# Performance work log

Hardware: AMD Instinct MI355X
Metric: run time of the kernel (lower is better)

Reference implementation:

```python
import jax, jax.numpy as jnp
import numpy as np

D_MODEL = 1024
EXPAND = 2
INNER = D_MODEL * EXPAND  # 2048
D_STATE = 64
K = 3
BSZ = 2
SEQ = 4096


def setup_inputs() -> dict:
    key = jax.random.key(0)
    ks = jax.random.split(key, 12)
    s = 0.02

    def w(k, shape):
        return jax.random.normal(k, shape, jnp.float32) * s

    return {
        "x": jax.random.normal(ks[0], (BSZ, SEQ, D_MODEL), jnp.float32),
        "W_in": w(ks[1], (D_MODEL, 2 * INNER)),
        "b_in": jnp.zeros((2 * INNER,), jnp.float32),
        "conv_w": w(ks[2], (INNER, K)),            # depthwise kernel per channel
        "conv_b": jnp.zeros((INNER,), jnp.float32),
        "W_dt": w(ks[3], (INNER, D_STATE)),
        "b_dt": jnp.zeros((D_STATE,), jnp.float32),
        "W_B": w(ks[4], (INNER, D_STATE)),
        "b_B": jnp.zeros((D_STATE,), jnp.float32),
        "W_C": w(ks[5], (INNER, D_STATE)),
        "b_C": jnp.zeros((D_STATE,), jnp.float32),
        "W_si": w(ks[6], (D_STATE, INNER)),
        "b_si": jnp.zeros((INNER,), jnp.float32),
        "D": jnp.ones((INNER,), jnp.float32),
        "W_out": w(ks[7], (INNER, D_MODEL)),
        "b_out": jnp.zeros((D_MODEL,), jnp.float32),
    }


def reference(x, W_in, b_in, conv_w, conv_b, W_dt, b_dt, W_B, b_B, W_C, b_C,
              W_si, b_si, D, W_out, b_out):
    bsz, seq_len, _ = x.shape
    inner = W_in.shape[1] // 2
    k = conv_w.shape[1]

    xz = x @ W_in + b_in                      # [B, L, 2*inner]
    x_main, gate = xz[..., :inner], xz[..., inner:]

    # Causal depthwise conv: torch pads k-1 both sides then slices [:L],
    # equivalent to left-pad (k-1), right-pad 0.
    lhs = jnp.transpose(x_main, (0, 2, 1))    # [B, C, L]
    rhs = conv_w[:, None, :]                  # [C, 1, K]
    conv = jax.lax.conv_general_dilated(
        lhs, rhs, window_strides=(1,), padding=[(k - 1, 0)],
        dimension_numbers=("NCH", "OIH", "NCH"), feature_group_count=inner)
    x_main = jnp.transpose(conv, (0, 2, 1)) + conv_b  # [B, L, inner]
    x_main = jax.nn.silu(x_main)

    dt = jax.nn.sigmoid(x_main @ W_dt + b_dt)  # [B, L, d_state]
    Bm = x_main @ W_B + b_B
    Cm = x_main @ W_C + b_C

    # Selective state recurrence: state_t = (1-dt_t)*state_{t-1} + dt_t*B_t
    def step(state, inp):
        dt_t, B_t, C_t = inp                  # each [B, d_state]
        state = (1.0 - dt_t) * state + dt_t * B_t
        return state, C_t * state

    xs = (jnp.moveaxis(dt, 1, 0), jnp.moveaxis(Bm, 1, 0), jnp.moveaxis(Cm, 1, 0))
    state0 = jnp.zeros((bsz, dt.shape[-1]), x.dtype)
    _, y = jax.lax.scan(step, state0, xs)     # [L, B, d_state]
    y = jnp.moveaxis(y, 0, 1)                 # [B, L, d_state]

    # LayerNorm over last dim, no affine, eps=1e-5 (torch F.layer_norm default)
    mu = jnp.mean(y, axis=-1, keepdims=True)
    var = jnp.var(y, axis=-1, keepdims=True)
    y = (y - mu) * jax.lax.rsqrt(var + 1e-5)

    y = y @ W_si + b_si                       # [B, L, inner]
    y = y + D * x_main
    y = y * jax.nn.sigmoid(gate)
    return y @ W_out + b_out                  # [B, L, d_model]
```

## Files before the change

### kernel.cpp

```cpp
#include <hip/hip_runtime.h>
#include <hip/hip_bf16.h>
#include <math.h>


namespace {

typedef __bf16 bf16x8 __attribute__((ext_vector_type(8)));
typedef float  f32x4  __attribute__((ext_vector_type(4)));
typedef unsigned short u16;

constexpr int kSeq = 4096;

__device__ __forceinline__ float sigmoid_f(float x) { return 1.0f / (1.0f + expf(-x)); }
__device__ __forceinline__ u16   f2bf(float f) { __bf16 h = (__bf16)f; return __builtin_bit_cast(u16, h); }
__device__ __forceinline__ float bf2f(u16 u)   { return (float)__builtin_bit_cast(__bf16, u); }

__device__ __forceinline__ void gll16(const u16* g, u16* l) {
    __builtin_amdgcn_global_load_lds(
        (const __attribute__((address_space(1))) unsigned int*)g,
        (__attribute__((address_space(3))) unsigned int*)l,
        16, 0, 0);
}

__device__ __forceinline__ int xcd_swizzle(int lin, int nwg) {
    const int q = nwg >> 3, r = nwg & 7;
    const int xcd = lin & 7, idx = lin >> 3;
    return (xcd < r ? xcd * (q + 1) : r * (q + 1) + (xcd - r) * q) + idx;
}

__global__ __launch_bounds__(256)
void convert_bf16(const float* __restrict__ in, u16* __restrict__ out, long n4)
{
    long i = (long)blockIdx.x * 256 + threadIdx.x;
    if (i >= n4) return;
    float4 v = reinterpret_cast<const float4*>(in)[i];
    ushort4 o = make_ushort4(f2bf(v.x), f2bf(v.y), f2bf(v.z), f2bf(v.w));
    reinterpret_cast<ushort4*>(out)[i] = o;
}

__device__ __forceinline__ void tr_body(float (*tile)[33],
                                        const float* __restrict__ in, u16* __restrict__ out,
                                        int R, int C, int r0, int c0, int t)
{
    const int lr = t >> 3, lc = (t & 7) * 4;
    float4 v = *reinterpret_cast<const float4*>(in + (size_t)(r0 + lr) * C + c0 + lc);
    tile[lr][lc + 0] = v.x; tile[lr][lc + 1] = v.y;
    tile[lr][lc + 2] = v.z; tile[lr][lc + 3] = v.w;
    __syncthreads();
    const int oc = t >> 3, orr = (t & 7) * 4;
    ushort4 o = make_ushort4(f2bf(tile[orr + 0][oc]), f2bf(tile[orr + 1][oc]),
                             f2bf(tile[orr + 2][oc]), f2bf(tile[orr + 3][oc]));
    *reinterpret_cast<ushort4*>(out + (size_t)(c0 + oc) * R + r0 + orr) = o;
}

__global__ __launch_bounds__(256)
void transpose_big(const float* __restrict__ Win, u16* __restrict__ WinT,
                   const float* __restrict__ Wout, u16* __restrict__ WoutT)
{
    __shared__ float tile[32][33];
    const int t = threadIdx.x;
    if (blockIdx.z == 0) {
        tr_body(tile, Win, WinT, 1024, 4096, blockIdx.y * 32, blockIdx.x * 32, t);
    } else {
        if (blockIdx.x >= 64) return;
        tr_body(tile, Wout, WoutT, 2048, 1024, blockIdx.x * 32, blockIdx.y * 32, t);
    }
}

__global__ __launch_bounds__(256)
void transpose_small(const float* __restrict__ Wdt, const float* __restrict__ WB,
                     const float* __restrict__ WC,  const float* __restrict__ Wsi,
                     u16* __restrict__ WdtbcT, u16* __restrict__ WsiT)
{
    __shared__ float tile[32][33];
    const int t = threadIdx.x;
    const int z = blockIdx.z;
    if (z < 3) {
        const float* in = (z == 0) ? Wdt : (z == 1) ? WB : WC;
        u16* out = WdtbcT + (size_t)z * 64 * 2048;
        tr_body(tile, in, out, 2048, 64, blockIdx.y * 32, blockIdx.x * 32, t);
    } else {
        tr_body(tile, Wsi, WsiT, 64, 2048, blockIdx.x * 32, blockIdx.y * 32, t);
    }
}

template <int BM, int BN, int EPI>
__global__ __launch_bounds__(256)
void gemm_mfma(const u16* __restrict__ A, const u16* __restrict__ Bt,
               const float* __restrict__ b0, const float* __restrict__ b1,
               const float* __restrict__ b2,
               const u16* __restrict__ aux0, const u16* __restrict__ aux1,
               void* __restrict__ o0, int N, int K, int nbx)
{
    constexpr int FM = BM / 32, FN = BN / 32;
    constexpr int CA = BM / 32, CB = BN / 32;
    __shared__ __align__(16) u16 As[BM][64];
    __shared__ __align__(16) u16 Bs[BN][64];

    const int tid  = threadIdx.x;
    const int lane = tid & 63;
    const int wid  = tid >> 6;
    const int wr   = (wid >> 1) * (BM / 2);
    const int wc   = (wid & 1)  * (BN / 2);
    const int swz  = xcd_swizzle(blockIdx.x, gridDim.x);
    const int row0 = (swz / nbx) * BM;
    const int col0 = (swz % nbx) * BN;

    const int srow = lane >> 3;
    const int scol = ((lane & 7) ^ srow) * 8;
    const int fr   = lane & 15;
    const int fq   = lane >> 4;

    f32x4 acc[FM][FN];
#pragma unroll
    for (int m = 0; m < FM; ++m)
#pragma unroll
        for (int n = 0; n < FN; ++n) acc[m][n] = (f32x4){0.f, 0.f, 0.f, 0.f};

    for (int k0 = 0; k0 < K; k0 += 64) {
#pragma unroll
        for (int i = 0; i < CA; ++i) {
            const int c = wid * CA + i;
            gll16(A + (size_t)(row0 + c * 8 + srow) * K + k0 + scol,
                  &As[0][0] + c * 512 + lane * 8);
        }
#pragma unroll
        for (int i = 0; i < CB; ++i) {
            const int c = wid * CB + i;
            gll16(Bt + (size_t)(col0 + c * 8 + srow) * K + k0 + scol,
                  &Bs[0][0] + c * 512 + lane * 8);
        }
        __syncthreads();
#pragma unroll
        for (int kk = 0; kk < 2; ++kk) {
            bf16x8 af[FM], bg[FN];
#pragma unroll
            for (int m = 0; m < FM; ++m) {
                const int rr = wr + m * 16 + fr;
                af[m] = *reinterpret_cast<const bf16x8*>(
                    &As[rr][(kk * 32 + fq * 8) ^ ((rr & 7) * 8)]);
            }
#pragma unroll
            for (int n = 0; n < FN; ++n) {
                const int rr = wc + n * 16 + fr;
                bg[n] = *reinterpret_cast<const bf16x8*>(
                    &Bs[rr][(kk * 32 + fq * 8) ^ ((rr & 7) * 8)]);
            }
#pragma unroll
            for (int m = 0; m < FM; ++m)
#pragma unroll
                for (int n = 0; n < FN; ++n)
                    acc[m][n] = __builtin_amdgcn_mfma_f32_16x16x32_bf16(af[m], bg[n], acc[m][n], 0, 0, 0);
        }
        __syncthreads();
    }

#pragma unroll
    for (int m = 0; m < FM; ++m) {
#pragma unroll
        for (int n = 0; n < FN; ++n) {
            const int gc  = col0 + wc + n * 16 + fr;
            const int gr0 = row0 + wr + m * 16 + fq * 4;
            if constexpr (EPI == 2) {
                float4 vv;
                float* vp = (float*)&vv;
#pragma unroll
                for (int j = 0; j < 4; ++j) {
                    float bb = (gc < 64) ? b0[gc] : (gc < 128) ? b1[gc - 64] : b2[gc - 128];
                    float v = acc[m][n][j] + bb;
                    if (gc < 64) v = sigmoid_f(v);
                    vp[j] = v;
                }
                *reinterpret_cast<float4*>(&((float*)o0)[(size_t)gc * 8192 + gr0]) = vv;
            } else {
#pragma unroll
                for (int j = 0; j < 4; ++j) {
                    const int gr = gr0 + j;
                    float v = acc[m][n][j];
                    if constexpr (EPI == 0) {
                        ((float*)o0)[(size_t)gr * N + gc] = v + b0[gc];
                    } else if constexpr (EPI == 1) {
                        ((u16*)o0)[(size_t)gr * N + gc] = f2bf(v + b0[gc]);
                    } else {
                        const size_t p = (size_t)gr * 2048 + gc;
                        float g  = bf2f(aux0[(size_t)gr * 4096 + gc]);
                        float xa = bf2f(aux1[p]);
                        v = v + b0[gc] + b1[gc] * xa;
                        ((u16*)o0)[p] = f2bf(v * sigmoid_f(g));
                    }
                }
            }
        }
    }
    (void)b1; (void)b2; (void)aux0; (void)aux1;
}

__global__ __launch_bounds__(256)
void conv_silu(const u16* __restrict__ xz, const float* __restrict__ cw,
               const float* __restrict__ cb, u16* __restrict__ xact)
{
    const size_t g  = ((size_t)blockIdx.x * 256 + threadIdx.x) * 8;
    const int    c0 = (int)(g & 2047);
    const size_t r  = g >> 11;
    const int    s  = (int)(r & (kSeq - 1));
    const u16* p = xz + r * 4096 + c0;
    u16 X0[8], X1[8] = {}, X2[8] = {};
    *reinterpret_cast<uint4*>(X0) = *reinterpret_cast<const uint4*>(p);
    if (s >= 1) *reinterpret_cast<uint4*>(X1) = *reinterpret_cast<const uint4*>(p - 4096);
    if (s >= 2) *reinterpret_cast<uint4*>(X2) = *reinterpret_cast<const uint4*>(p - 8192);
    u16 O[8];
#pragma unroll
    for (int j = 0; j < 8; ++j) {
        const int c = c0 + j;
        float v = bf2f(X2[j]) * cw[c * 3 + 0] + bf2f(X1[j]) * cw[c * 3 + 1]
                + bf2f(X0[j]) * cw[c * 3 + 2] + cb[c];
        O[j] = f2bf(v * sigmoid_f(v));
    }
    *reinterpret_cast<uint4*>(xact + r * 2048 + c0) = *reinterpret_cast<uint4*>(O);
}

__global__ __launch_bounds__(256)
void scan_kernel(const float* __restrict__ dtbcT, float* __restrict__ y)
{
    const int b = blockIdx.x >> 6;
    const int d = blockIdx.x & 63;
    const int t = threadIdx.x;
    const int lane = t & 63;
    const int w = t >> 6;
    const size_t col = (size_t)b * kSeq + t * 16;
    const float* dtp = dtbcT + (size_t)d         * 8192 + col;
    const float* Bp  = dtbcT + (size_t)(64 + d)  * 8192 + col;
    const float* Cp  = dtbcT + (size_t)(128 + d) * 8192 + col;

    float av[16], bv[16];
    float Acc = 1.f, Bcc = 0.f;
#pragma unroll
    for (int q = 0; q < 4; ++q) {
        float4 dv = *reinterpret_cast<const float4*>(dtp + q * 4);
        float4 Bv = *reinterpret_cast<const float4*>(Bp + q * 4);
        const float* dvp = (const float*)&dv;
        const float* bvp = (const float*)&Bv;
#pragma unroll
        for (int j = 0; j < 4; ++j) {
            const int i = q * 4 + j;
            float a  = 1.f - dvp[j];
            float bb = dvp[j] * bvp[j];
            av[i] = a; bv[i] = bb;
            Acc = a * Acc;
            Bcc = a * Bcc + bb;
        }
    }

#pragma unroll
    for (int off = 1; off < 64; off <<= 1) {
        float pA = __shfl_up(Acc, off, 64);
        float pB = __shfl_up(Bcc, off, 64);
        if (lane >= off) { Bcc = Acc * pB + Bcc; Acc = Acc * pA; }
    }
    __shared__ float wA[4], wB[4];
    if (lane == 63) { wA[w] = Acc; wB[w] = Bcc; }
    float eA = __shfl_up(Acc, 1, 64);
    float eB = __shfl_up(Bcc, 1, 64);
    if (lane == 0) { eA = 1.f; eB = 0.f; }
    __syncthreads();
    float sW = 0.f;
    for (int i = 0; i < w; ++i) sW = wA[i] * sW + wB[i];
    float s = eA * sW + eB;

#pragma unroll
    for (int q = 0; q < 4; ++q) {
        float4 Cv = *reinterpret_cast<const float4*>(Cp + q * 4);
        const float* cvp = (const float*)&Cv;
#pragma unroll
        for (int j = 0; j < 4; ++j) {
            const int i = q * 4 + j;
            s = av[i] * s + bv[i];
            y[(col + i) * 64 + d] = cvp[j] * s;
        }
    }
}

__global__ __launch_bounds__(256)
void ln_kernel(const float* __restrict__ y, u16* __restrict__ ynb)
{
    const int w = threadIdx.x >> 6;
    const int l = threadIdx.x & 63;
    const size_t r = (size_t)blockIdx.x * 4 + w;
    float v  = y[r * 64 + l];
    float s  = v, s2 = v * v;
#pragma unroll
    for (int m = 1; m < 64; m <<= 1) {
        s  += __shfl_xor(s, m, 64);
        s2 += __shfl_xor(s2, m, 64);
    }
    float mu  = s * (1.f / 64.f);
    float var = s2 * (1.f / 64.f) - mu * mu;
    ynb[r * 64 + l] = f2bf((v - mu) * rsqrtf(var + 1e-5f));
}

}

extern "C" void kernel_launch(void* const* d_in, const int* in_sizes, int n_in,
                              void* d_out, int out_size, void* d_ws, size_t ws_size,
                              hipStream_t stream)
{
    (void)in_sizes; (void)n_in; (void)out_size; (void)ws_size;
    const float* x     = (const float*)d_in[0];
    const float* W_in  = (const float*)d_in[1];
    const float* b_in  = (const float*)d_in[2];
    const float* cw    = (const float*)d_in[3];
    const float* cb    = (const float*)d_in[4];
    const float* W_dt  = (const float*)d_in[5];
    const float* b_dt  = (const float*)d_in[6];
    const float* W_B   = (const float*)d_in[7];
    const float* b_B   = (const float*)d_in[8];
    const float* W_C   = (const float*)d_in[9];
    const float* b_C   = (const float*)d_in[10];
    const float* W_si  = (const float*)d_in[11];
    const float* b_si  = (const float*)d_in[12];
    const float* Dv    = (const float*)d_in[13];
    const float* W_out = (const float*)d_in[14];
    const float* b_out = (const float*)d_in[15];
    float* out = (float*)d_out;

    char* ws = (char*)d_ws;
    u16*   xzb    = (u16*)  (ws);
    u16*   xb     = (u16*)  (ws + 67108864);
    u16*   xact   = (u16*)  (ws + 83886080);
    u16*   hb     = (u16*)  (ws + 117440512);
    float* dtbcT  = (float*)(ws + 150994944);
    float* ybuf   = (float*)(ws + 157286400);
    u16*   ynb    = (u16*)  (ws + 159383552);
    u16*   WinT   = (u16*)  (ws + 160432128);
    u16*   WoutT  = (u16*)  (ws + 168820736);
    u16*   WdtbcT = (u16*)  (ws + 173015040);
    u16*   WsiT   = (u16*)  (ws + 173801472);

    dim3 blk(256);

    convert_bf16<<<dim3((8192L * 1024 / 4 + 255) / 256), blk, 0, stream>>>(x, xb, 8192L * 1024 / 4);
    transpose_big<<<dim3(128, 32, 2), blk, 0, stream>>>(W_in, WinT, W_out, WoutT);
    transpose_small<<<dim3(2, 64, 4), blk, 0, stream>>>(W_dt, W_B, W_C, W_si, WdtbcT, WsiT);

    gemm_mfma<128, 128, 1><<<dim3(32 * 64), blk, 0, stream>>>(
        xb, WinT, b_in, nullptr, nullptr, nullptr, nullptr, xzb, 4096, 1024, 32);
    conv_silu<<<dim3(8192L * 2048 / (8 * 256)), blk, 0, stream>>>(xzb, cw, cb, xact);
    gemm_mfma<32, 192, 2><<<dim3(256), blk, 0, stream>>>(
        xact, WdtbcT, b_dt, b_B, b_C, nullptr, nullptr, dtbcT, 192, 2048, 1);
    scan_kernel<<<dim3(128), blk, 0, stream>>>(dtbcT, ybuf);
    ln_kernel<<<dim3(8192 / 4), blk, 0, stream>>>(ybuf, ynb);
    gemm_mfma<128, 128, 3><<<dim3(16 * 64), blk, 0, stream>>>(
        ynb, WsiT, b_si, Dv, nullptr, xzb + 2048, xact, hb, 2048, 64, 16);
    gemm_mfma<128, 128, 0><<<dim3(8 * 64), blk, 0, stream>>>(
        hb, WoutT, b_out, nullptr, nullptr, nullptr, nullptr, out, 1024, 2048, 8);
}
```

Before: 246.7 us.

## Stage GEMM epilogues through LDS for coalesced vector stores; retile dt/B/C GEMM

The 128x128 GEMM epilogues now write accumulators to a padded shared-memory tile in two halves, then each thread reads a contiguous row segment and issues vectorized float4/uint4 global stores and aux loads, instead of scattered per-element stores from the MFMA fragment layout. The shared buffer is unioned with the A/B staging tiles so LDS usage does not grow. Separately, the dt/B/C projection GEMM is retiled from 32x192 blocks (256 blocks) to 64x64 blocks (384 blocks) to raise parallelism. The staging adds extra barriers and LDS traffic per block.

Measured after the change: 277.3 us. +12.4%, slower.

```diff
diff --git a/kernel.cpp b/kernel.cpp
--- a/kernel.cpp
+++ b/kernel.cpp
@@ -94,8 +94,12 @@
 {
     constexpr int FM = BM / 32, FN = BN / 32;
     constexpr int CA = BM / 32, CB = BN / 32;
-    __shared__ __align__(16) u16 As[BM][64];
-    __shared__ __align__(16) u16 Bs[BN][64];
+    constexpr int SM_STAGE = (BM + BN) * 64 * 2;
+    constexpr int SM_CS    = (EPI == 2) ? 0 : 64 * 129 * 4;
+    constexpr int SM_BYTES = SM_STAGE > SM_CS ? SM_STAGE : SM_CS;
+    __shared__ __align__(16) char smem[SM_BYTES];
+    u16* As = (u16*)smem;
+    u16* Bs = As + BM * 64;
 
     const int tid  = threadIdx.x;
     const int lane = tid & 63;
@@ -122,13 +126,13 @@
         for (int i = 0; i < CA; ++i) {
             const int c = wid * CA + i;
             gll16(A + (size_t)(row0 + c * 8 + srow) * K + k0 + scol,
-                  &As[0][0] + c * 512 + lane * 8);
+                  As + c * 512 + lane * 8);
         }
 #pragma unroll
         for (int i = 0; i < CB; ++i) {
             const int c = wid * CB + i;
             gll16(Bt + (size_t)(col0 + c * 8 + srow) * K + k0 + scol,
-                  &Bs[0][0] + c * 512 + lane * 8);
+                  Bs + c * 512 + lane * 8);
         }
         __syncthreads();
 #pragma unroll
@@ -138,13 +142,13 @@
             for (int m = 0; m < FM; ++m) {
                 const int rr = wr + m * 16 + fr;
                 af[m] = *reinterpret_cast<const bf16x8*>(
-                    &As[rr][(kk * 32 + fq * 8) ^ ((rr & 7) * 8)]);
+                    As + rr * 64 + ((kk * 32 + fq * 8) ^ ((rr & 7) * 8)));
             }
 #pragma unroll
             for (int n = 0; n < FN; ++n) {
                 const int rr = wc + n * 16 + fr;
                 bg[n] = *reinterpret_cast<const bf16x8*>(
-                    &Bs[rr][(kk * 32 + fq * 8) ^ ((rr & 7) * 8)]);
+                    Bs + rr * 64 + ((kk * 32 + fq * 8) ^ ((rr & 7) * 8)));
             }
 #pragma unroll
             for (int m = 0; m < FM; ++m)
@@ -155,13 +159,13 @@
         __syncthreads();
     }
 
-#pragma unroll
-    for (int m = 0; m < FM; ++m) {
-#pragma unroll
-        for (int n = 0; n < FN; ++n) {
-            const int gc  = col0 + wc + n * 16 + fr;
-            const int gr0 = row0 + wr + m * 16 + fq * 4;
-            if constexpr (EPI == 2) {
+    if constexpr (EPI == 2) {
+#pragma unroll
+        for (int m = 0; m < FM; ++m) {
+#pragma unroll
+            for (int n = 0; n < FN; ++n) {
+                const int gc  = col0 + wc + n * 16 + fr;
+                const int gr0 = row0 + wr + m * 16 + fq * 4;
                 float4 vv;
                 float* vp = (float*)&vv;
 #pragma unroll
@@ -172,22 +176,67 @@
                     vp[j] = v;
                 }
                 *reinterpret_cast<float4*>(&((float*)o0)[(size_t)gc * 8192 + gr0]) = vv;
+            }
+        }
+    } else {
+        static_assert(EPI == 2 || (BM == 128 && BN == 128), "transpose epi needs 128x128");
+        float* Cs = (float*)smem;
+        const int rrow = tid >> 2;
+        const int rc   = (tid & 3) * 32;
+#pragma unroll
+        for (int h = 0; h < 2; ++h) {
+            if (h == 1) __syncthreads();
+            if ((wid >> 1) == h) {
+#pragma unroll
+                for (int m = 0; m < FM; ++m)
+#pragma unroll
+                    for (int n = 0; n < FN; ++n)
+#pragma unroll
+                        for (int j = 0; j < 4; ++j)
+                            Cs[(m * 16 + fq * 4 + j) * 129 + wc + n * 16 + fr] = acc[m][n][j];
+            }
+            __syncthreads();
+            const int gr  = row0 + h * 64 + rrow;
+            const int gc0 = col0 + rc;
+            float v[32];
+#pragma unroll
+            for (int i = 0; i < 8; ++i)
+                *reinterpret_cast<float4*>(&v[i * 4]) =
+                    *reinterpret_cast<const float4*>(&Cs[rrow * 129 + rc + i * 4]);
+            if constexpr (EPI == 0) {
+#pragma unroll
+                for (int i = 0; i < 8; ++i) {
+                    float4 bb = *reinterpret_cast<const float4*>(&b0[gc0 + i * 4]);
+                    float4 o = make_float4(v[i * 4 + 0] + bb.x, v[i * 4 + 1] + bb.y,
+                                           v[i * 4 + 2] + bb.z, v[i * 4 + 3] + bb.w);
+                    *reinterpret_cast<float4*>(&((float*)o0)[(size_t)gr * N + gc0 + i * 4]) = o;
+                }
+            } else if constexpr (EPI == 1) {
+#pragma unroll
+                for (int q = 0; q < 4; ++q) {
+                    u16 o[8];
+#pragma unroll
+                    for (int i = 0; i < 8; ++i)
+                        o[i] = f2bf(v[q * 8 + i] + b0[gc0 + q * 8 + i]);
+                    *reinterpret_cast<uint4*>(&((u16*)o0)[(size_t)gr * N + gc0 + q * 8]) =
+                        *reinterpret_cast<const uint4*>(o);
+                }
             } else {
 #pragma unroll
-                for (int j = 0; j < 4; ++j) {
-                    const int gr = gr0 + j;
-                    float v = acc[m][n][j];
-                    if constexpr (EPI == 0) {
-                        ((float*)o0)[(size_t)gr * N + gc] = v + b0[gc];
-                    } else if constexpr (EPI == 1) {
-                        ((u16*)o0)[(size_t)gr * N + gc] = f2bf(v + b0[gc]);
-                    } else {
-                        const size_t p = (size_t)gr * 2048 + gc;
-                        float g  = bf2f(aux0[(size_t)gr * 4096 + gc]);
-                        float xa = bf2f(aux1[p]);
-                        v = v + b0[gc] + b1[gc] * xa;
-                        ((u16*)o0)[p] = f2bf(v * sigmoid_f(g));
+                for (int q = 0; q < 4; ++q) {
+                    u16 gv[8], xv[8], o[8];
+                    *reinterpret_cast<uint4*>(gv) =
+                        *reinterpret_cast<const uint4*>(&aux0[(size_t)gr * 4096 + gc0 + q * 8]);
+                    *reinterpret_cast<uint4*>(xv) =
+                        *reinterpret_cast<const uint4*>(&aux1[(size_t)gr * 2048 + gc0 + q * 8]);
+#pragma unroll
+                    for (int i = 0; i < 8; ++i) {
+                        const int c = gc0 + q * 8 + i;
+                        float val = v[q * 8 + i] + b0[c] + b1[c] * bf2f(xv[i]);
+                        o[i] = f2bf(val * sigmoid_f(bf2f(gv[i])));
                     }
+                    *reinterpret_cast<uint4*>(&((u16*)o0)[(size_t)gr * 2048 + gc0 + q * 8]) =
+                        *reinterpret_cast<const uint4*>(o);
                 }
             }
         }
@@ -345,8 +394,8 @@
     gemm_mfma<128, 128, 1><<<dim3(32 * 64), blk, 0, stream>>>(
         xb, WinT, b_in, nullptr, nullptr, nullptr, nullptr, xzb, 4096, 1024, 32);
     conv_silu<<<dim3(8192L * 2048 / (8 * 256)), blk, 0, stream>>>(xzb, cw, cb, xact);
-    gemm_mfma<32, 192, 2><<<dim3(256), blk, 0, stream>>>(
-        xact, WdtbcT, b_dt, b_B, b_C, nullptr, nullptr, dtbcT, 192, 2048, 1);
+    gemm_mfma<64, 64, 2><<<dim3(3 * 128), blk, 0, stream>>>(
+        xact, WdtbcT, b_dt, b_B, b_C, nullptr, nullptr, dtbcT, 192, 2048, 3);
     scan_kernel<<<dim3(128), blk, 0, stream>>>(dtbcT, ybuf);
     ln_kernel<<<dim3(8192 / 4), blk, 0, stream>>>(ybuf, ynb);
     gemm_mfma<128, 128, 3><<<dim3(16 * 64), blk, 0, stream>>>(
```
